# Optimization experiments

Measured on AMD Instinct MI355X. Metric: run time of the kernel, lower is better.

The kernel has to match this reference:

```python
import jax, jax.numpy as jnp
import numpy as np

D = 768
N_HEAD = 12
HEAD_D = D // N_HEAD


def setup_inputs() -> dict:
    key = jax.random.key(0)
    ks = jax.random.split(key, 9)
    s = 1.0 / np.sqrt(D)
    inp = {
        "x": jax.random.normal(ks[0], (2, 2048, D), dtype=jnp.float32),
        "Wq": jax.random.normal(ks[1], (D, D), dtype=jnp.float32) * s,
        "bq": jnp.zeros((D,), dtype=jnp.float32),
        "Wk": jax.random.normal(ks[2], (D, D), dtype=jnp.float32) * s,
        "bk": jnp.zeros((D,), dtype=jnp.float32),
        "Wv": jax.random.normal(ks[3], (D, D), dtype=jnp.float32) * s,
        "bv": jnp.zeros((D,), dtype=jnp.float32),
        "Wo": jax.random.normal(ks[4], (D, D), dtype=jnp.float32) * s,
        "bo": jnp.zeros((D,), dtype=jnp.float32),
    }
    return inp


def reference(x, Wq, bq, Wk, bk, Wv, bv, Wo, bo):
    B, S, _ = x.shape
    # projections; split heads -> [B, H, S, hd]
    def heads(t):
        return t.reshape(B, S, N_HEAD, HEAD_D).transpose(0, 2, 1, 3)
    q = heads(x @ Wq.T + bq)
    k = heads(x @ Wk.T + bk)
    v = heads(x @ Wv.T + bv)
    scale = 1.0 / np.sqrt(HEAD_D)
    scores = jnp.einsum("bhqd,bhkd->bhqk", q, k) * scale  # [B,H,S,S]
    causal = jnp.tril(jnp.ones((S, S), dtype=bool))
    scores = jnp.where(causal, scores, jnp.float32(-jnp.inf))
    attn = jax.nn.softmax(scores, axis=-1)
    out = jnp.einsum("bhqk,bhkd->bhqd", attn, v)
    out = out.transpose(0, 2, 1, 3).reshape(B, S, D)
    return out @ Wo.T + bo
```

## Files before the change

### kernel.cpp

```cpp
#include <hip/hip_runtime.h>
#include <hip/hip_bf16.h>

#define BD 2
#define SLEN 2048
#define DDIM 768
#define HNUM 12
#define HD 64
#define MROWS (BD * SLEN)

using short4v = __attribute__((ext_vector_type(4))) short;
using short8 = __attribute__((ext_vector_type(8))) short;
using f32x4 = __attribute__((ext_vector_type(4))) float;
using uint4v = __attribute__((ext_vector_type(4))) unsigned int;

__device__ __forceinline__ short f2bf(float f) {
  __hip_bfloat16 h = __float2bfloat16(f);
  return *reinterpret_cast<short*>(&h);
}
__device__ __forceinline__ float bf2f(short s) {
  unsigned int u = ((unsigned int)(unsigned short)s) << 16;
  float f;
  __builtin_memcpy(&f, &u, 4);
  return f;
}
__device__ __forceinline__ unsigned pkbf(float a, float b) {
  return (unsigned)(unsigned short)f2bf(a) |
         ((unsigned)(unsigned short)f2bf(b) << 16);
}

#define P_ELEM ((size_t)MROWS * DDIM)
#define PW_ELEM ((size_t)DDIM * DDIM)

__global__ __launch_bounds__(256) void cvt_split(
    const float* __restrict__ x, const float* __restrict__ Wq,
    const float* __restrict__ Wk, const float* __restrict__ Wv,
    const float* __restrict__ Wo, short* __restrict__ ws) {
  const float* src;
  short* hi;
  size_t n;
  switch (blockIdx.z) {
    case 0:  src = x;  hi = ws;                             n = P_ELEM;  break;
    case 1:  src = Wq; hi = ws + 2 * P_ELEM;                n = PW_ELEM; break;
    case 2:  src = Wk; hi = ws + 2 * P_ELEM + 2 * PW_ELEM;  n = PW_ELEM; break;
    case 3:  src = Wv; hi = ws + 2 * P_ELEM + 4 * PW_ELEM;  n = PW_ELEM; break;
    default: src = Wo; hi = ws + 2 * P_ELEM + 6 * PW_ELEM;  n = PW_ELEM; break;
  }
  short* lo = hi + n;
  const size_t n4 = n >> 2;
  for (size_t i = (size_t)blockIdx.x * 256 + threadIdx.x; i < n4;
       i += (size_t)gridDim.x * 256) {
    float4 f = ((const float4*)src)[i];
    short4v h, l;
    h[0] = f2bf(f.x); h[1] = f2bf(f.y); h[2] = f2bf(f.z); h[3] = f2bf(f.w);
    l[0] = f2bf(f.x - bf2f(h[0]));
    l[1] = f2bf(f.y - bf2f(h[1]));
    l[2] = f2bf(f.z - bf2f(h[2]));
    l[3] = f2bf(f.w - bf2f(h[3]));
    ((short4v*)hi)[i] = h;
    ((short4v*)lo)[i] = l;
  }
}

template <int BM, int BN, int MODE>
__device__ __forceinline__ void gemm3_body(
    const short* __restrict__ Ah, const short* __restrict__ Al,
    const short* __restrict__ Bh, const short* __restrict__ Bl,
    const float* __restrict__ bias, float scale, void* __restrict__ outp) {
  __shared__ short As[2][BM][32];
  __shared__ short Bs[2][BN][32];

  const int n0 = blockIdx.x * BN;
  const int m0 = blockIdx.y * BM;
  const int t = threadIdx.x;
  const int w = t >> 6, l = t & 63;
  const int wm = w >> 1, wn = w & 1;
  const int x = l & 15, g = l >> 4;

  constexpr int NI = BM / 32, NJ = BN / 32;
  constexpr int QA = BM / 64;
  constexpr int QB = BN / 64;
  constexpr int PER = 2 * QA + 2 * QB;

  f32x4 acc[NI][NJ];
  #pragma unroll
  for (int i = 0; i < NI; ++i)
    #pragma unroll
    for (int j = 0; j < NJ; ++j) acc[i][j] = (f32x4){0.f, 0.f, 0.f, 0.f};

  short8 rg[PER];
  auto load_chunks = [&](int k0) {
    #pragma unroll
    for (int q = 0; q < PER; ++q) {
      const short* gp;
      int rowbase, local;
      if (q < QA)               { gp = Ah; rowbase = m0; local = q * 256 + t; }
      else if (q < 2 * QA)      { gp = Al; rowbase = m0; local = (q - QA) * 256 + t; }
      else if (q < 2 * QA + QB) { gp = Bh; rowbase = n0; local = (q - 2 * QA) * 256 + t; }
      else                      { gp = Bl; rowbase = n0; local = (q - 2 * QA - QB) * 256 + t; }
      rg[q] = *(const short8*)(gp + (size_t)(rowbase + (local >> 2)) * DDIM +
                               k0 + (local & 3) * 8);
    }
  };

  load_chunks(0);
  for (int k0 = 0; k0 < DDIM; k0 += 32) {
    __syncthreads();
    #pragma unroll
    for (int q = 0; q < PER; ++q) {
      short* lp;
      int local;
      if (q < QA)               { lp = &As[0][0][0]; local = q * 256 + t; }
      else if (q < 2 * QA)      { lp = &As[1][0][0]; local = (q - QA) * 256 + t; }
      else if (q < 2 * QA + QB) { lp = &Bs[0][0][0]; local = (q - 2 * QA) * 256 + t; }
      else                      { lp = &Bs[1][0][0]; local = (q - 2 * QA - QB) * 256 + t; }
      *(short8*)(lp + local * 8) = rg[q];
    }
    if (k0 + 32 < DDIM) load_chunks(k0 + 32);
    __syncthreads();

    short8 af[2][NI], bf[2][NJ];
    #pragma unroll
    for (int i = 0; i < NI; ++i) {
      af[0][i] = *(const short8*)&As[0][wm * (BM / 2) + i * 16 + x][8 * g];
      af[1][i] = *(const short8*)&As[1][wm * (BM / 2) + i * 16 + x][8 * g];
    }
    #pragma unroll
    for (int j = 0; j < NJ; ++j) {
      bf[0][j] = *(const short8*)&Bs[0][wn * (BN / 2) + j * 16 + x][8 * g];
      bf[1][j] = *(const short8*)&Bs[1][wn * (BN / 2) + j * 16 + x][8 * g];
    }
    __builtin_amdgcn_s_setprio(1);
    #pragma unroll
    for (int i = 0; i < NI; ++i)
      #pragma unroll
      for (int j = 0; j < NJ; ++j) {
        acc[i][j] = __builtin_amdgcn_mfma_f32_16x16x32_bf16(af[0][i], bf[0][j], acc[i][j], 0, 0, 0);
        acc[i][j] = __builtin_amdgcn_mfma_f32_16x16x32_bf16(af[0][i], bf[1][j], acc[i][j], 0, 0, 0);
        acc[i][j] = __builtin_amdgcn_mfma_f32_16x16x32_bf16(af[1][i], bf[0][j], acc[i][j], 0, 0, 0);
      }
    __builtin_amdgcn_s_setprio(0);
  }

  #pragma unroll
  for (int j = 0; j < NJ; ++j) {
    const int n = n0 + wn * (BN / 2) + j * 16 + x;
    const float bj = bias[n];
    #pragma unroll
    for (int i = 0; i < NI; ++i) {
      #pragma unroll
      for (int reg = 0; reg < 4; ++reg) {
        const int m = m0 + wm * (BM / 2) + i * 16 + 4 * g + reg;
        const float v = (acc[i][j][reg] + bj) * scale;
        if (MODE == 0) {
          ((float*)outp)[(size_t)m * DDIM + n] = v;
        } else {
          const int b_ = m >> 11, s_ = m & (SLEN - 1);
          const int h_ = n >> 6, d_ = n & (HD - 1);
          ((short*)outp)[(((size_t)(b_ * HNUM + h_) * SLEN + s_) * HD) + d_] = f2bf(v);
        }
      }
    }
  }
}

__global__ __launch_bounds__(256) void gemm_qkv3(
    const short* __restrict__ ws, const float* __restrict__ bq,
    const float* __restrict__ bk, const float* __restrict__ bv,
    short* __restrict__ Qb, short* __restrict__ Kb, short* __restrict__ Vb) {
  const short* Ah = ws;
  const short* Al = ws + P_ELEM;
  const short* Bh;
  const float* bias;
  short* out;
  float scale;
  switch (blockIdx.z) {
    case 0:  Bh = ws + 2 * P_ELEM;                bias = bq; out = Qb; scale = 0.125f; break;
    case 1:  Bh = ws + 2 * P_ELEM + 2 * PW_ELEM;  bias = bk; out = Kb; scale = 1.f;   break;
    default: Bh = ws + 2 * P_ELEM + 4 * PW_ELEM;  bias = bv; out = Vb; scale = 1.f;   break;
  }
  gemm3_body<128, 128, 1>(Ah, Al, Bh, Bh + PW_ELEM, bias, scale, out);
}

__global__ __launch_bounds__(256) void gemm_out3(
    const short* __restrict__ AOh, const short* __restrict__ AOl,
    const short* __restrict__ Wh, const short* __restrict__ Wl,
    const float* __restrict__ bias, float* __restrict__ out) {
  gemm3_body<64, 64, 0>(AOh, AOl, Wh, Wl, bias, 1.f, out);
}

__global__ __launch_bounds__(256) void flash_fwd_mfma(
    const short* __restrict__ Q, const short* __restrict__ K,
    const short* __restrict__ V, short* __restrict__ AOh,
    short* __restrict__ AOl) {
  const int bh = blockIdx.x;
  const int qt = 31 - (int)blockIdx.y;
  const int b = bh / HNUM, h = bh % HNUM;
  const int t = threadIdx.x;
  const int w = t >> 6, l = t & 63;
  const int x = l & 15, g = l >> 4;
  const int q0 = qt * 64;
  const int qrow = q0 + 16 * w + x;

  __shared__ short Klds[128][72];
  __shared__ short Vlds[64][138];

  short8 Qf[2];
  {
    const short* qp = Q + ((size_t)bh * SLEN + qrow) * HD;
    Qf[0] = *(const short8*)(qp + 8 * g);
    Qf[1] = *(const short8*)(qp + 8 * g + 32);
  }

  f32x4 Oacc[4];
  #pragma unroll
  for (int dc = 0; dc < 4; ++dc) Oacc[dc] = (f32x4){0.f, 0.f, 0.f, 0.f};
  float m_run = -1e30f, l_run = 0.f;

  const int ntiles = qt / 2 + 1;

  short8 krg[4], vrg[4];
  auto load_tile = [&](int kt) {
    const size_t rowb = (size_t)bh * SLEN + (size_t)kt * 128;
    #pragma unroll
    for (int q = 0; q < 4; ++q) {
      const int c = q * 256 + t;
      krg[q] = *(const short8*)(K + (rowb + (c >> 3)) * HD + (c & 7) * 8);
      vrg[q] = *(const short8*)(V + (rowb + (c >> 3)) * HD + (c & 7) * 8);
    }
  };

  load_tile(0);
  for (int kt = 0; kt < ntiles; ++kt) {
    __syncthreads();
    #pragma unroll
    for (int q = 0; q < 4; ++q) {
      const int c = q * 256 + t;
      *(short8*)&Klds[c >> 3][(c & 7) * 8] = krg[q];
      const int j = c >> 3, d0 = (c & 7) * 8;
      #pragma unroll
      for (int i = 0; i < 8; ++i) Vlds[d0 + i][j] = vrg[q][i];
    }
    if (kt + 1 < ntiles) load_tile(kt + 1);
    __syncthreads();

    f32x4 S[8];
    __builtin_amdgcn_s_setprio(1);
    #pragma unroll
    for (int jt = 0; jt < 8; ++jt) {
      short8 Kf0 = *(const short8*)&Klds[16 * jt + x][8 * g];
      short8 Kf1 = *(const short8*)&Klds[16 * jt + x][8 * g + 32];
      f32x4 z = (f32x4){0.f, 0.f, 0.f, 0.f};
      z = __builtin_amdgcn_mfma_f32_16x16x32_bf16(Kf0, Qf[0], z, 0, 0, 0);
      S[jt] = __builtin_amdgcn_mfma_f32_16x16x32_bf16(Kf1, Qf[1], z, 0, 0, 0);
    }
    __builtin_amdgcn_s_setprio(0);

    if (kt == ntiles - 1) {
      const int jb = kt * 128 + 4 * g;
      #pragma unroll
      for (int jt = 0; jt < 8; ++jt)
        #pragma unroll
        for (int r = 0; r < 4; ++r)
          if (jb + 16 * jt + r > qrow) S[jt][r] = -1e30f;
    }

    float tm = -1e30f;
    #pragma unroll
    for (int jt = 0; jt < 8; ++jt)
      #pragma unroll
      for (int r = 0; r < 4; ++r) tm = fmaxf(tm, S[jt][r]);
    tm = fmaxf(tm, __shfl_xor(tm, 16));
    tm = fmaxf(tm, __shfl_xor(tm, 32));
    const float mn = fmaxf(m_run, tm);
    const float resc = __expf(m_run - mn);
    m_run = mn;
    float ts = 0.f;
    #pragma unroll
    for (int jt = 0; jt < 8; ++jt)
      #pragma unroll
      for (int r = 0; r < 4; ++r) {
        const float p = __expf(S[jt][r] - mn);
        S[jt][r] = p;
        ts += p;
      }
    ts += __shfl_xor(ts, 16);
    ts += __shfl_xor(ts, 32);
    l_run = l_run * resc + ts;
    #pragma unroll
    for (int dc = 0; dc < 4; ++dc) Oacc[dc] *= resc;

    uint4v PA[4];
    const bool hihalf = (g >= 2);
    const bool oddg = (g & 1);
    #pragma unroll
    for (int c = 0; c < 4; ++c) {
      const unsigned e_lo = pkbf(S[2 * c][0], S[2 * c][1]);
      const unsigned e_hi = pkbf(S[2 * c][2], S[2 * c][3]);
      const unsigned o_lo = pkbf(S[2 * c + 1][0], S[2 * c + 1][1]);
      const unsigned o_hi = pkbf(S[2 * c + 1][2], S[2 * c + 1][3]);
      const unsigned xe_lo = (unsigned)__shfl_xor((int)e_lo, 32);
      const unsigned xe_hi = (unsigned)__shfl_xor((int)e_hi, 32);
      const unsigned xo_lo = (unsigned)__shfl_xor((int)o_lo, 32);
      const unsigned xo_hi = (unsigned)__shfl_xor((int)o_hi, 32);
      const unsigned ap_lo = hihalf ? xo_lo : e_lo;
      const unsigned ap_hi = hihalf ? xo_hi : e_hi;
      const unsigned bp_lo = hihalf ? o_lo : xe_lo;
      const unsigned bp_hi = hihalf ? o_hi : xe_hi;
      const unsigned sa_lo = (unsigned)__shfl_xor((int)ap_lo, 16);
      const unsigned sa_hi = (unsigned)__shfl_xor((int)ap_hi, 16);
      const unsigned sb_lo = (unsigned)__shfl_xor((int)bp_lo, 16);
      const unsigned sb_hi = (unsigned)__shfl_xor((int)bp_hi, 16);
      PA[c][0] = oddg ? sb_lo : ap_lo;
      PA[c][1] = oddg ? sb_hi : ap_hi;
      PA[c][2] = oddg ? bp_lo : sa_lo;
      PA[c][3] = oddg ? bp_hi : sa_hi;
    }

    __builtin_amdgcn_s_setprio(1);
    #pragma unroll
    for (int dc = 0; dc < 4; ++dc) {
      #pragma unroll
      for (int c = 0; c < 4; ++c) {
        short8 Vf = *(const short8*)&Vlds[16 * dc + x][32 * c + 8 * g];
        Oacc[dc] = __builtin_amdgcn_mfma_f32_16x16x32_bf16(
            Vf, *(const short8*)&PA[c], Oacc[dc], 0, 0, 0);
      }
    }
    __builtin_amdgcn_s_setprio(0);
  }

  const float inv = 1.f / l_run;
  const size_t base = ((size_t)(b * SLEN + qrow)) * DDIM + h * HD + 4 * g;
  #pragma unroll
  for (int dc = 0; dc < 4; ++dc) {
    short4v hi4, lo4;
    #pragma unroll
    for (int r = 0; r < 4; ++r) {
      const float v = Oacc[dc][r] * inv;
      const short hh = f2bf(v);
      hi4[r] = hh;
      lo4[r] = f2bf(v - bf2f(hh));
    }
    *(short4v*)(AOh + base + 16 * dc) = hi4;
    *(short4v*)(AOl + base + 16 * dc) = lo4;
  }
}

extern "C" void kernel_launch(void* const* d_in, const int* in_sizes, int n_in,
                              void* d_out, int out_size, void* d_ws, size_t ws_size,
                              hipStream_t stream) {
  const float* x  = (const float*)d_in[0];
  const float* Wq = (const float*)d_in[1];
  const float* bq = (const float*)d_in[2];
  const float* Wk = (const float*)d_in[3];
  const float* bk = (const float*)d_in[4];
  const float* Wv = (const float*)d_in[5];
  const float* bv = (const float*)d_in[6];
  const float* Wo = (const float*)d_in[7];
  const float* bo = (const float*)d_in[8];
  float* out = (float*)d_out;

  short* S = (short*)d_ws;
  short* AOh = S;
  short* AOl = S + P_ELEM;
  const short* Wo_h = S + 2 * P_ELEM + 6 * PW_ELEM;
  const short* Wo_l = Wo_h + PW_ELEM;
  short* Qb = S + 2 * P_ELEM + 8 * PW_ELEM;
  short* Kb = Qb + P_ELEM;
  short* Vb = Kb + P_ELEM;

  dim3 blk(256);
  cvt_split<<<dim3(768, 1, 5), blk, 0, stream>>>(x, Wq, Wk, Wv, Wo, S);
  gemm_qkv3<<<dim3(DDIM / 128, MROWS / 128, 3), blk, 0, stream>>>(
      S, bq, bk, bv, Qb, Kb, Vb);
  flash_fwd_mfma<<<dim3(BD * HNUM, SLEN / 64), blk, 0, stream>>>(
      Qb, Kb, Vb, AOh, AOl);
  gemm_out3<<<dim3(DDIM / 64, MROWS / 64), blk, 0, stream>>>(
      AOh, AOl, Wo_h, Wo_l, bo, out);
}
```

Baseline: 222.4 us.

## Load GEMM A-fragments directly from global into registers, bypassing LDS

The GEMM body no longer stages the A operand (hi/lo activation splits) through shared memory. Each wave loads its MFMA A-fragments straight from global memory into registers, double-buffered one k-step ahead, while B still goes through LDS. This halves LDS traffic and shared-memory footprint and drops one set of LDS writes and reads per k-step. In exchange each A row is fetched redundantly by the two waves sharing it (wn=0/1), global loads are less coalesced (16-byte chunks at row stride), register pressure rises, and launch bounds now request 2 blocks per CU.

```diff
diff --git a/kernel.cpp b/kernel.cpp
--- a/kernel.cpp
+++ b/kernel.cpp
@@ -66,7 +66,6 @@
     const short* __restrict__ Ah, const short* __restrict__ Al,
     const short* __restrict__ Bh, const short* __restrict__ Bl,
     const float* __restrict__ bias, float scale, void* __restrict__ outp) {
-  __shared__ short As[2][BM][32];
   __shared__ short Bs[2][BN][32];
 
   const int n0 = blockIdx.x * BN;
@@ -77,9 +76,8 @@
   const int x = l & 15, g = l >> 4;
 
   constexpr int NI = BM / 32, NJ = BN / 32;
-  constexpr int QA = BM / 64;
   constexpr int QB = BN / 64;
-  constexpr int PER = 2 * QA + 2 * QB;
+  constexpr int PERB = 2 * QB;
 
   f32x4 acc[NI][NJ];
   #pragma unroll
@@ -87,58 +85,67 @@
     #pragma unroll
     for (int j = 0; j < NJ; ++j) acc[i][j] = (f32x4){0.f, 0.f, 0.f, 0.f};
 
-  short8 rg[PER];
-  auto load_chunks = [&](int k0) {
-    #pragma unroll
-    for (int q = 0; q < PER; ++q) {
-      const short* gp;
-      int rowbase, local;
-      if (q < QA)               { gp = Ah; rowbase = m0; local = q * 256 + t; }
-      else if (q < 2 * QA)      { gp = Al; rowbase = m0; local = (q - QA) * 256 + t; }
-      else if (q < 2 * QA + QB) { gp = Bh; rowbase = n0; local = (q - 2 * QA) * 256 + t; }
-      else                      { gp = Bl; rowbase = n0; local = (q - 2 * QA - QB) * 256 + t; }
-      rg[q] = *(const short8*)(gp + (size_t)(rowbase + (local >> 2)) * DDIM +
-                               k0 + (local & 3) * 8);
+  size_t aoff[NI];
+  #pragma unroll
+  for (int i = 0; i < NI; ++i)
+    aoff[i] = (size_t)(m0 + wm * (BM / 2) + i * 16 + x) * DDIM + 8 * g;
+
+  short8 brg[PERB];
+  auto loadB = [&](int k0) {
+    #pragma unroll
+    for (int q = 0; q < PERB; ++q) {
+      const short* gp = (q < QB) ? Bh : Bl;
+      const int local = (q % QB) * 256 + t;
+      brg[q] = *(const short8*)(gp + (size_t)(n0 + (local >> 2)) * DDIM +
+                                k0 + (local & 3) * 8);
     }
   };
 
-  load_chunks(0);
-  for (int k0 = 0; k0 < DDIM; k0 += 32) {
+  short8 afA[2][NI], afB[2][NI];
+#define LOADA(dst, k0)                                       \
+  _Pragma("unroll")                                          \
+  for (int i_ = 0; i_ < NI; ++i_) {                          \
+    dst[0][i_] = *(const short8*)(Ah + aoff[i_] + (k0));     \
+    dst[1][i_] = *(const short8*)(Al + aoff[i_] + (k0));     \
+  }
+
+  LOADA(afA, 0);
+  loadB(0);
+
+  auto step = [&](int k0, short8 (&afU)[2][NI], short8 (&afP)[2][NI]) {
     __syncthreads();
     #pragma unroll
-    for (int q = 0; q < PER; ++q) {
-      short* lp;
-      int local;
-      if (q < QA)               { lp = &As[0][0][0]; local = q * 256 + t; }
-      else if (q < 2 * QA)      { lp = &As[1][0][0]; local = (q - QA) * 256 + t; }
-      else if (q < 2 * QA + QB) { lp = &Bs[0][0][0]; local = (q - 2 * QA) * 256 + t; }
-      else                      { lp = &Bs[1][0][0]; local = (q - 2 * QA - QB) * 256 + t; }
-      *(short8*)(lp + local * 8) = rg[q];
-    }
-    if (k0 + 32 < DDIM) load_chunks(k0 + 32);
+    for (int q = 0; q < PERB; ++q) {
+      short* lp = (q < QB) ? &Bs[0][0][0] : &Bs[1][0][0];
+      const int local = (q % QB) * 256 + t;
+      *(short8*)(lp + local * 8) = brg[q];
+    }
+    if (k0 + 32 < DDIM) loadB(k0 + 32);
     __syncthreads();
 
-    short8 af[2][NI], bf[2][NJ];
-    #pragma unroll
-    for (int i = 0; i < NI; ++i) {
-      af[0][i] = *(const short8*)&As[0][wm * (BM / 2) + i * 16 + x][8 * g];
-      af[1][i] = *(const short8*)&As[1][wm * (BM / 2) + i * 16 + x][8 * g];
-    }
+    short8 bf[2][NJ];
     #pragma unroll
     for (int j = 0; j < NJ; ++j) {
       bf[0][j] = *(const short8*)&Bs[0][wn * (BN / 2) + j * 16 + x][8 * g];
       bf[1][j] = *(const short8*)&Bs[1][wn * (BN / 2) + j * 16 + x][8 * g];
     }
+    const int kn = (k0 + 32 < DDIM) ? (k0 + 32) : 0;
+    LOADA(afP, kn);
     __builtin_amdgcn_s_setprio(1);
     #pragma unroll
     for (int i = 0; i < NI; ++i)
       #pragma unroll
       for (int j = 0; j < NJ; ++j) {
-        acc[i][j] = __builtin_amdgcn_mfma_f32_16x16x32_bf16(af[0][i], bf[0][j], acc[i][j], 0, 0, 0);
-        acc[i][j] = __builtin_amdgcn_mfma_f32_16x16x32_bf16(af[0][i], bf[1][j], acc[i][j], 0, 0, 0);
-        acc[i][j] = __builtin_amdgcn_mfma_f32_16x16x32_bf16(af[1][i], bf[0][j], acc[i][j], 0, 0, 0);
+        acc[i][j] = __builtin_amdgcn_mfma_f32_16x16x32_bf16(afU[0][i], bf[0][j], acc[i][j], 0, 0, 0);
+        acc[i][j] = __builtin_amdgcn_mfma_f32_16x16x32_bf16(afU[0][i], bf[1][j], acc[i][j], 0, 0, 0);
+        acc[i][j] = __builtin_amdgcn_mfma_f32_16x16x32_bf16(afU[1][i], bf[0][j], acc[i][j], 0, 0, 0);
       }
     __builtin_amdgcn_s_setprio(0);
+  };
+
+  for (int kk = 0; kk < DDIM; kk += 64) {
+    step(kk, afA, afB);
+    step(kk + 32, afB, afA);
   }
 
   #pragma unroll
@@ -161,9 +168,10 @@
       }
     }
   }
-}
-
-__global__ __launch_bounds__(256) void gemm_qkv3(
+#undef LOADA
+}
+
+__global__ __launch_bounds__(256, 2) void gemm_qkv3(
     const short* __restrict__ ws, const float* __restrict__ bq,
     const float* __restrict__ bk, const float* __restrict__ bv,
     short* __restrict__ Qb, short* __restrict__ Kb, short* __restrict__ Vb) {
@@ -181,7 +189,7 @@
   gemm3_body<128, 128, 1>(Ah, Al, Bh, Bh + PW_ELEM, bias, scale, out);
 }
 
-__global__ __launch_bounds__(256) void gemm_out3(
+__global__ __launch_bounds__(256, 2) void gemm_out3(
     const short* __restrict__ AOh, const short* __restrict__ AOl,
     const short* __restrict__ Wh, const short* __restrict__ Wl,
     const float* __restrict__ bias, float* __restrict__ out) {
```

Measured after the change: 263.5 us. 1.18x slower.

## Stage GEMM tiles straight into swizzled double-buffered LDS with async loads

Applied to the files above, without the earlier changes.

The split-bf16 GEMM body now uses global_load_lds to copy A and B tiles straight from global memory into LDS, skipping the register round-trip. LDS is double-buffered so the next k-slice streams in while the current one feeds the MFMAs, and one barrier per iteration is removed. An XOR swizzle on the 16-byte chunk index is applied on both write and read to cut LDS bank conflicts. Launch bounds ask for two blocks per CU, but the doubled LDS footprint may limit occupancy for the 128x128 tile.

```diff
diff --git a/kernel.cpp b/kernel.cpp
--- a/kernel.cpp
+++ b/kernel.cpp
@@ -26,6 +26,11 @@
 __device__ __forceinline__ unsigned pkbf(float a, float b) {
   return (unsigned)(unsigned short)f2bf(a) |
          ((unsigned)(unsigned short)f2bf(b) << 16);
+}
+__device__ __forceinline__ void gload16(const short* g, short* l) {
+  __builtin_amdgcn_global_load_lds(
+      (const __attribute__((address_space(1))) unsigned int*)g,
+      (__attribute__((address_space(3))) unsigned int*)l, 16, 0, 0);
 }
 
 #define P_ELEM ((size_t)MROWS * DDIM)
@@ -66,8 +71,8 @@
     const short* __restrict__ Ah, const short* __restrict__ Al,
     const short* __restrict__ Bh, const short* __restrict__ Bl,
     const float* __restrict__ bias, float scale, void* __restrict__ outp) {
-  __shared__ short As[2][BM][32];
-  __shared__ short Bs[2][BN][32];
+  __shared__ short As[2][2][BM][32];
+  __shared__ short Bs[2][2][BN][32];
 
   const int n0 = blockIdx.x * BN;
   const int m0 = blockIdx.y * BM;
@@ -79,7 +84,6 @@
   constexpr int NI = BM / 32, NJ = BN / 32;
   constexpr int QA = BM / 64;
   constexpr int QB = BN / 64;
-  constexpr int PER = 2 * QA + 2 * QB;
 
   f32x4 acc[NI][NJ];
   #pragma unroll
@@ -87,47 +91,49 @@
     #pragma unroll
     for (int j = 0; j < NJ; ++j) acc[i][j] = (f32x4){0.f, 0.f, 0.f, 0.f};
 
-  short8 rg[PER];
-  auto load_chunks = [&](int k0) {
-    #pragma unroll
-    for (int q = 0; q < PER; ++q) {
-      const short* gp;
-      int rowbase, local;
-      if (q < QA)               { gp = Ah; rowbase = m0; local = q * 256 + t; }
-      else if (q < 2 * QA)      { gp = Al; rowbase = m0; local = (q - QA) * 256 + t; }
-      else if (q < 2 * QA + QB) { gp = Bh; rowbase = n0; local = (q - 2 * QA) * 256 + t; }
-      else                      { gp = Bl; rowbase = n0; local = (q - 2 * QA - QB) * 256 + t; }
-      rg[q] = *(const short8*)(gp + (size_t)(rowbase + (local >> 2)) * DDIM +
-                               k0 + (local & 3) * 8);
+  auto stage = [&](int bb, int k0) {
+    #pragma unroll
+    for (int q = 0; q < QA; ++q) {
+      const int local = q * 256 + t;
+      const int row = local >> 2;
+      const int ks = (local & 3) ^ ((row >> 1) & 3);
+      const int lbase = (q * 256 + (t & 192)) * 8;
+      const size_t go = (size_t)(m0 + row) * DDIM + k0 + ks * 8;
+      gload16(Ah + go, &As[bb][0][0][0] + lbase);
+      gload16(Al + go, &As[bb][1][0][0] + lbase);
+    }
+    #pragma unroll
+    for (int q = 0; q < QB; ++q) {
+      const int local = q * 256 + t;
+      const int row = local >> 2;
+      const int ks = (local & 3) ^ ((row >> 1) & 3);
+      const int lbase = (q * 256 + (t & 192)) * 8;
+      const size_t go = (size_t)(n0 + row) * DDIM + k0 + ks * 8;
+      gload16(Bh + go, &Bs[bb][0][0][0] + lbase);
+      gload16(Bl + go, &Bs[bb][1][0][0] + lbase);
     }
   };
 
-  load_chunks(0);
+  stage(0, 0);
+  int cur = 0;
   for (int k0 = 0; k0 < DDIM; k0 += 32) {
     __syncthreads();
-    #pragma unroll
-    for (int q = 0; q < PER; ++q) {
-      short* lp;
-      int local;
-      if (q < QA)               { lp = &As[0][0][0]; local = q * 256 + t; }
-      else if (q < 2 * QA)      { lp = &As[1][0][0]; local = (q - QA) * 256 + t; }
-      else if (q < 2 * QA + QB) { lp = &Bs[0][0][0]; local = (q - 2 * QA) * 256 + t; }
-      else                      { lp = &Bs[1][0][0]; local = (q - 2 * QA - QB) * 256 + t; }
-      *(short8*)(lp + local * 8) = rg[q];
-    }
-    if (k0 + 32 < DDIM) load_chunks(k0 + 32);
-    __syncthreads();
+    if (k0 + 32 < DDIM) stage(cur ^ 1, k0 + 32);
 
     short8 af[2][NI], bf[2][NJ];
     #pragma unroll
     for (int i = 0; i < NI; ++i) {
-      af[0][i] = *(const short8*)&As[0][wm * (BM / 2) + i * 16 + x][8 * g];
-      af[1][i] = *(const short8*)&As[1][wm * (BM / 2) + i * 16 + x][8 * g];
+      const int row = wm * (BM / 2) + i * 16 + x;
+      const int ks = g ^ ((row >> 1) & 3);
+      af[0][i] = *(const short8*)&As[cur][0][row][ks * 8];
+      af[1][i] = *(const short8*)&As[cur][1][row][ks * 8];
     }
     #pragma unroll
     for (int j = 0; j < NJ; ++j) {
-      bf[0][j] = *(const short8*)&Bs[0][wn * (BN / 2) + j * 16 + x][8 * g];
-      bf[1][j] = *(const short8*)&Bs[1][wn * (BN / 2) + j * 16 + x][8 * g];
+      const int row = wn * (BN / 2) + j * 16 + x;
+      const int ks = g ^ ((row >> 1) & 3);
+      bf[0][j] = *(const short8*)&Bs[cur][0][row][ks * 8];
+      bf[1][j] = *(const short8*)&Bs[cur][1][row][ks * 8];
     }
     __builtin_amdgcn_s_setprio(1);
     #pragma unroll
@@ -139,6 +145,7 @@
         acc[i][j] = __builtin_amdgcn_mfma_f32_16x16x32_bf16(af[1][i], bf[0][j], acc[i][j], 0, 0, 0);
       }
     __builtin_amdgcn_s_setprio(0);
+    cur ^= 1;
   }
 
   #pragma unroll
@@ -163,7 +170,7 @@
   }
 }
 
-__global__ __launch_bounds__(256) void gemm_qkv3(
+__global__ __launch_bounds__(256, 2) void gemm_qkv3(
     const short* __restrict__ ws, const float* __restrict__ bq,
     const float* __restrict__ bk, const float* __restrict__ bv,
     short* __restrict__ Qb, short* __restrict__ Kb, short* __restrict__ Vb) {
@@ -181,7 +188,7 @@
   gemm3_body<128, 128, 1>(Ah, Al, Bh, Bh + PW_ELEM, bias, scale, out);
 }
 
-__global__ __launch_bounds__(256) void gemm_out3(
+__global__ __launch_bounds__(256, 2) void gemm_out3(
     const short* __restrict__ AOh, const short* __restrict__ AOl,
     const short* __restrict__ Wh, const short* __restrict__ Wl,
     const float* __restrict__ bias, float* __restrict__ out) {
```

Measured after the change: 222.4 us. About the same (+0.0%).
